# Kernel tuning notes

Measured on AMD Instinct MI355X. Metric: run time of the kernel, lower is better.

Reference implementation:

```python
import jax, jax.numpy as jnp
import numpy as np

NX, NU, ND = 512, 128, 64
BATCH, T = 256, 256


def setup_inputs() -> dict:
    key = jax.random.key(0)
    ks = jax.random.split(key, 7)
    return {
        "x": jax.random.normal(ks[0], (BATCH, NX), dtype=jnp.float32),
        "U": jax.random.normal(ks[1], (T, BATCH, NU), dtype=jnp.float32),
        "D": jax.random.normal(ks[2], (T, BATCH, ND), dtype=jnp.float32),
        "A_weight": jax.random.normal(ks[3], (NX, NX), dtype=jnp.float32),
        "A_scalar": jax.random.normal(ks[4], (NX, NX), dtype=jnp.float32),
        "B_weight": jax.random.normal(ks[5], (NX, NU), dtype=jnp.float32) * 0.05,
        "E_weight": jax.random.normal(ks[6], (NX, ND), dtype=jnp.float32) * 0.05,
    }


def _effective_W(weight, scalar):
    # (1 - 0.1*sigmoid(scalar)) * softmax(weight, axis=1), then transposed
    s_clamped = 1.0 - 0.1 * jax.nn.sigmoid(scalar)
    return (s_clamped * jax.nn.softmax(weight, axis=1)).T  # [nx, nx]


def reference(x, U, D, A_weight, A_scalar, B_weight, E_weight):
    W_eff = _effective_W(A_weight, A_scalar)            # hoisted: constant over time
    # Precompute input injections: [T, batch, nx]
    inj = jnp.einsum('tbu,xu->tbx', U, B_weight) + jnp.einsum('tbd,xd->tbx', D, E_weight)

    def step(x_prev, inj_t):
        x_new = x_prev @ W_eff + inj_t
        return x_new, x_new

    _, X = jax.lax.scan(step, x, inj)                   # X: [T, batch, nx]
    Y = X[:, :, -1]                                     # [T, batch]
    return X, Y
```

## Files before the change

kernel.cpp:

```cpp
#include <hip/hip_runtime.h>
#include <hip/hip_bf16.h>
#include <cstddef>

#define NXX 512
#define NUU 128
#define NDD 64
#define BB  256
#define TT  256
#define CL  8
#define NC  32
#define BS  (BB * NXX)
#define MS  (NXX * NXX)
#define LDK 32

typedef __attribute__((ext_vector_type(8))) short short8;
typedef __attribute__((ext_vector_type(8))) unsigned short ushort8;
typedef __attribute__((ext_vector_type(4))) unsigned short ushort4v;
typedef __attribute__((ext_vector_type(4))) float f32x4;

__device__ __forceinline__ unsigned short f2bf(float f) {
    union { float f; unsigned u; } v; v.f = f;
    unsigned r = v.u + 0x7FFFu + ((v.u >> 16) & 1u);
    return (unsigned short)(r >> 16);
}
__device__ __forceinline__ float bf2f(unsigned short h) {
    union { unsigned u; float f; } v; v.u = ((unsigned)h) << 16;
    return v.f;
}

enum StageKind { SK_BF16_NAT, SK_BF16_TRANS };

template<StageKind SK>
__device__ __forceinline__ void stage_tile(const void* src, int ld, int r0, int k0,
                                           unsigned short (*S)[LDK])
{
    const int tid = threadIdx.x;
    if constexpr (SK == SK_BF16_NAT) {
        const unsigned short* s = (const unsigned short*)src;
        const int wave = tid >> 6, lane = tid & 63;
#pragma unroll
        for (int i = 0; i < 2; ++i) {
            int rb = wave * 16 + i * 64;
            int r  = rb + (lane >> 2);
            int c  = (lane & 3) << 3;
            const unsigned short* g = s + (size_t)(r0 + r) * ld + k0 + c;
            __builtin_amdgcn_global_load_lds(
                (const __attribute__((address_space(1))) void*)g,
                (__attribute__((address_space(3))) void*)&S[rb][0],
                16, 0, 0);
        }
    } else {
        const unsigned short* s = (const unsigned short*)src;
#pragma unroll
        for (int i = 0; i < 2; ++i) {
            int idx = tid + i * 256;
            int m   = idx >> 4;
            int c   = (idx & 15) << 3;
            ushort8 v = *(const ushort8*)(s + (size_t)(k0 + m) * ld + r0 + c);
#pragma unroll
            for (int j = 0; j < 8; ++j) S[c + j][m] = v[j];
        }
    }
}

template<StageKind AK, StageKind BK>
__device__ __forceinline__ void gemm_mainloop(
    f32x4 (&acc)[4][4],
    const void* A, int lda, const void* B, int ldb,
    int K, int row0, int n0,
    unsigned short (*As)[LDK], unsigned short (*Bs)[LDK])
{
    const int tid  = threadIdx.x;
    const int lane = tid & 63;
    const int wave = tid >> 6;
    const int wm   = (wave >> 1) * 64;
    const int wn   = (wave & 1) * 64;
    const int l16  = lane & 15;
    const int quad = lane >> 4;

    for (int k0 = 0; k0 < K; k0 += 32) {
        __syncthreads();
        stage_tile<AK>(A, lda, row0, k0, As);
        stage_tile<BK>(B, ldb, n0,   k0, Bs);
        __syncthreads();
        short8 af[4], bfr[4];
#pragma unroll
        for (int f = 0; f < 4; ++f)
            af[f] = *(const short8*)&As[wm + f * 16 + l16][quad * 8];
#pragma unroll
        for (int f = 0; f < 4; ++f)
            bfr[f] = *(const short8*)&Bs[wn + f * 16 + l16][quad * 8];
#pragma unroll
        for (int fm = 0; fm < 4; ++fm)
#pragma unroll
            for (int fn = 0; fn < 4; ++fn)
                acc[fm][fn] = __builtin_amdgcn_mfma_f32_16x16x32_bf16(
                    af[fm], bfr[fn], acc[fm][fn], 0, 0, 0);
    }
}

__global__ __launch_bounds__(256) void k_weff(
    const float* __restrict__ Aw, const float* __restrict__ Asc,
    unsigned short* __restrict__ T1)
{
    const int n   = blockIdx.x;
    const int tid = threadIdx.x;
    const int lane = tid & 63, wave = tid >> 6;
    float v0 = Aw[(size_t)n * NXX + tid];
    float v1 = Aw[(size_t)n * NXX + 256 + tid];
    __shared__ float sred[4];
    float m = fmaxf(v0, v1);
#pragma unroll
    for (int off = 32; off; off >>= 1) m = fmaxf(m, __shfl_down(m, off));
    if (lane == 0) sred[wave] = m;
    __syncthreads();
    if (tid == 0) sred[0] = fmaxf(fmaxf(sred[0], sred[1]), fmaxf(sred[2], sred[3]));
    __syncthreads();
    const float mm = sred[0];
    __syncthreads();
    float e0 = expf(v0 - mm), e1 = expf(v1 - mm);
    float s = e0 + e1;
#pragma unroll
    for (int off = 32; off; off >>= 1) s += __shfl_down(s, off);
    if (lane == 0) sred[wave] = s;
    __syncthreads();
    if (tid == 0) sred[0] = sred[0] + sred[1] + sred[2] + sred[3];
    __syncthreads();
    const float inv = 1.0f / sred[0];
    float sc0 = 1.0f - 0.1f * (1.0f / (1.0f + expf(-Asc[(size_t)n * NXX + tid])));
    float sc1 = 1.0f - 0.1f * (1.0f / (1.0f + expf(-Asc[(size_t)n * NXX + 256 + tid])));
    unsigned short* out = T1 + (size_t)n * NXX;
    out[tid]       = f2bf(sc0 * e0 * inv);
    out[tid + 256] = f2bf(sc1 * e1 * inv);
}

__global__ __launch_bounds__(256) void k_prep(
    const float* __restrict__ Bw, const float* __restrict__ Ew,
    const float* __restrict__ x,
    unsigned short* __restrict__ Bwb, unsigned short* __restrict__ Ewb,
    unsigned short* __restrict__ G0)
{
    int i = (blockIdx.x * 256 + threadIdx.x) * 4;
    const float* src; unsigned short* dst; int k;
    if (i < 65536)       { src = Bw; dst = Bwb; k = i; }
    else if (i < 98304)  { src = Ew; dst = Ewb; k = i - 65536; }
    else                 { src = x;  dst = G0;  k = i - 98304; }
    float4 v = *(const float4*)(src + k);
    ushort4v h = { f2bf(v.x), f2bf(v.y), f2bf(v.z), f2bf(v.w) };
    *(ushort4v*)(dst + k) = h;
}

__global__ __launch_bounds__(256) void k_mulN(unsigned short* __restrict__ powb,
                                              int4 ns, int4 ts, int4 ds)
{
    const int z = blockIdx.z;
    const int an = (z == 0) ? ns.x : (z == 1) ? ns.y : (z == 2) ? ns.z : ns.w;
    const int at = (z == 0) ? ts.x : (z == 1) ? ts.y : (z == 2) ? ts.z : ts.w;
    const int ad = (z == 0) ? ds.x : (z == 1) ? ds.y : (z == 2) ? ds.z : ds.w;
    const unsigned short* A = powb + (size_t)an * MS;
    const unsigned short* B = powb + (size_t)at * MS;
    unsigned short*       D = powb + (size_t)ad * MS;
    __shared__ unsigned short As[128][LDK];
    __shared__ unsigned short Bs2[128][LDK];
    f32x4 acc[4][4] = {};
    const int row0 = blockIdx.y * 128, n0 = blockIdx.x * 128;
    gemm_mainloop<SK_BF16_NAT, SK_BF16_TRANS>(acc, A, NXX, B, NXX, NXX, row0, n0, As, Bs2);
    const int tid = threadIdx.x;
    const int lane = tid & 63, wave = tid >> 6;
    const int wm = (wave >> 1) * 64, wn = (wave & 1) * 64;
    const int l16 = lane & 15, quad = lane >> 4;
#pragma unroll
    for (int fm = 0; fm < 4; ++fm)
#pragma unroll
        for (int fn = 0; fn < 4; ++fn)
#pragma unroll
            for (int r = 0; r < 4; ++r) {
                int m = row0 + wm + fm * 16 + quad * 4 + r;
                int n = n0 + wn + fn * 16 + l16;
                D[(size_t)m * NXX + n] = f2bf(acc[fm][fn][r]);
            }
}

__global__ __launch_bounds__(256) void k_hs(
    const unsigned short* __restrict__ vsrc, unsigned short* __restrict__ vdst,
    const unsigned short* __restrict__ Am, int s)
{
    const int c = blockIdx.z;
    const int row0 = blockIdx.y * 128, n0 = blockIdx.x * 128;
    const int tid = threadIdx.x;
    if (c < s) {
        const unsigned short* sp = vsrc + (size_t)c * BS;
        unsigned short*       dp = vdst + (size_t)c * BS;
#pragma unroll
        for (int i = 0; i < 8; ++i) {
            int idx = tid + i * 256;
            int r = idx >> 4, cc = (idx & 15) << 3;
            *(ushort8*)(dp + (size_t)(row0 + r) * NXX + n0 + cc) =
                *(const ushort8*)(sp + (size_t)(row0 + r) * NXX + n0 + cc);
        }
        return;
    }
    __shared__ unsigned short As[128][LDK];
    __shared__ unsigned short Bs2[128][LDK];
    f32x4 acc[4][4] = {};
    gemm_mainloop<SK_BF16_NAT, SK_BF16_NAT>(acc, vsrc + (size_t)(c - s) * BS, NXX,
                                            Am, NXX, NXX, row0, n0, As, Bs2);
    const int lane = tid & 63, wave = tid >> 6;
    const int wm = (wave >> 1) * 64, wn = (wave & 1) * 64;
    const int l16 = lane & 15, quad = lane >> 4;
    const unsigned short* Cp = vsrc + (size_t)c * BS;
    unsigned short*       Dp = vdst + (size_t)c * BS;
#pragma unroll
    for (int fm = 0; fm < 4; ++fm)
#pragma unroll
        for (int fn = 0; fn < 4; ++fn)
#pragma unroll
            for (int r = 0; r < 4; ++r) {
                int m = row0 + wm + fm * 16 + quad * 4 + r;
                int n = n0 + wn + fn * 16 + l16;
                float v = acc[fm][fn][r] + bf2f(Cp[(size_t)m * NXX + n]);
                Dp[(size_t)m * NXX + n] = f2bf(v);
            }
}

__global__ __launch_bounds__(256) void k_xcorr(
    const unsigned short* __restrict__ vA, const unsigned short* __restrict__ powb,
    float* __restrict__ X, float* __restrict__ Y)
{
    const int t = blockIdx.z;
    const int c = t >> 3, j = t & 7;
    const int row0 = blockIdx.y * 128, n0 = blockIdx.x * 128;
    __shared__ unsigned short As[128][LDK];
    __shared__ unsigned short Bs2[128][LDK];
    f32x4 acc[4][4] = {};
    gemm_mainloop<SK_BF16_NAT, SK_BF16_NAT>(acc, vA + (size_t)c * BS, NXX,
                                            powb + (size_t)j * MS, NXX, NXX,
                                            row0, n0, As, Bs2);
    const int tid = threadIdx.x;
    const int lane = tid & 63, wave = tid >> 6;
    const int wm = (wave >> 1) * 64, wn = (wave & 1) * 64;
    const int l16 = lane & 15, quad = lane >> 4;
    float* Xt = X + (size_t)t * BB * NXX;
#pragma unroll
    for (int fm = 0; fm < 4; ++fm)
#pragma unroll
        for (int fn = 0; fn < 4; ++fn)
#pragma unroll
            for (int r = 0; r < 4; ++r) {
                int m = row0 + wm + fm * 16 + quad * 4 + r;
                int n = n0 + wn + fn * 16 + l16;
                float v = acc[fm][fn][r] + Xt[(size_t)m * NXX + n];
                Xt[(size_t)m * NXX + n] = v;
                if (n == NXX - 1) Y[(size_t)t * BB + m] = v;
            }
}

__global__ __launch_bounds__(1024, 4) void k_scanA(
    const float* __restrict__ U, const float* __restrict__ Dm,
    const unsigned short* __restrict__ Bwb, const unsigned short* __restrict__ Ewb,
    const unsigned short* __restrict__ Wt,
    unsigned short* __restrict__ Gout,
    float* __restrict__ X)
{
    const int c   = blockIdx.x;
    const int r0  = blockIdx.y * 32;
    const int tid = threadIdx.x;
    const int lane = tid & 63, wave = tid >> 6;
    const int l16 = lane & 15, quad = lane >> 4;

    __shared__ unsigned short Sb[32][520];
    __shared__ unsigned short Ub[32][136];
    __shared__ unsigned short Db[32][72];

    int woff[2], bwoff[2], ewoff[2];
#pragma unroll
    for (int g = 0; g < 2; ++g) {
        int n = wave * 32 + g * 16 + l16;
        woff[g]  = n * NXX + quad * 8;
        bwoff[g] = n * NUU + quad * 8;
        ewoff[g] = n * NDD + quad * 8;
    }

    f32x4 acc[2][2];

    for (int j = 0; j < CL; ++j) {
        const int t = c * CL + j;
        {
            int row = tid >> 5;
            int uc  = (tid & 31) * 4;
            const float* up = U + ((size_t)t * BB + r0 + row) * NUU + uc;
            float4 a0 = *(const float4*)(up);
            ushort4v h0 = { f2bf(a0.x), f2bf(a0.y), f2bf(a0.z), f2bf(a0.w) };
            *(ushort4v*)&Ub[row][uc] = h0;
            int dc = (tid & 31) * 2;
            const float* dp = Dm + ((size_t)t * BB + r0 + row) * NDD + dc;
            float2 b0 = *(const float2*)(dp);
            unsigned pk = (unsigned)f2bf(b0.x) | ((unsigned)f2bf(b0.y) << 16);
            *(unsigned*)&Db[row][dc] = pk;
        }
        __syncthreads();

#pragma unroll
        for (int f = 0; f < 2; ++f)
#pragma unroll
            for (int g = 0; g < 2; ++g) acc[f][g] = (f32x4){0.f, 0.f, 0.f, 0.f};

#pragma unroll
        for (int kk = 0; kk < 4; ++kk) {
            short8 a0 = *(const short8*)&Ub[l16][kk * 32 + quad * 8];
            short8 a1 = *(const short8*)&Ub[16 + l16][kk * 32 + quad * 8];
#pragma unroll
            for (int g = 0; g < 2; ++g) {
                short8 b = *(const short8*)(Bwb + bwoff[g] + kk * 32);
                acc[0][g] = __builtin_amdgcn_mfma_f32_16x16x32_bf16(a0, b, acc[0][g], 0, 0, 0);
                acc[1][g] = __builtin_amdgcn_mfma_f32_16x16x32_bf16(a1, b, acc[1][g], 0, 0, 0);
            }
        }
#pragma unroll
        for (int kk = 0; kk < 2; ++kk) {
            short8 a0 = *(const short8*)&Db[l16][kk * 32 + quad * 8];
            short8 a1 = *(const short8*)&Db[16 + l16][kk * 32 + quad * 8];
#pragma unroll
            for (int g = 0; g < 2; ++g) {
                short8 b = *(const short8*)(Ewb + ewoff[g] + kk * 32);
                acc[0][g] = __builtin_amdgcn_mfma_f32_16x16x32_bf16(a0, b, acc[0][g], 0, 0, 0);
                acc[1][g] = __builtin_amdgcn_mfma_f32_16x16x32_bf16(a1, b, acc[1][g], 0, 0, 0);
            }
        }
        if (j > 0) {
#pragma unroll
            for (int kk = 0; kk < 16; ++kk) {
                short8 a0 = *(const short8*)&Sb[l16][kk * 32 + quad * 8];
                short8 a1 = *(const short8*)&Sb[16 + l16][kk * 32 + quad * 8];
#pragma unroll
                for (int g = 0; g < 2; ++g) {
                    short8 b = *(const short8*)(Wt + woff[g] + kk * 32);
                    acc[0][g] = __builtin_amdgcn_mfma_f32_16x16x32_bf16(a0, b, acc[0][g], 0, 0, 0);
                    acc[1][g] = __builtin_amdgcn_mfma_f32_16x16x32_bf16(a1, b, acc[1][g], 0, 0, 0);
                }
            }
        }
        __syncthreads();

#pragma unroll
        for (int f = 0; f < 2; ++f)
#pragma unroll
            for (int g = 0; g < 2; ++g) {
                int n = wave * 32 + g * 16 + l16;
#pragma unroll
                for (int rr = 0; rr < 4; ++rr) {
                    int mr = f * 16 + quad * 4 + rr;
                    float v = acc[f][g][rr];
                    unsigned short hb = f2bf(v);
                    Sb[mr][n] = hb;
                    X[((size_t)t * BB + r0 + mr) * NXX + n] = v;
                    if (j == CL - 1)
                        Gout[((size_t)(c + 1) * BB + r0 + mr) * NXX + n] = hb;
                }
            }
    }
}

extern "C" void kernel_launch(void* const* d_in, const int* in_sizes, int n_in,
                              void* d_out, int out_size, void* d_ws, size_t ws_size,
                              hipStream_t stream)
{
    const float* x   = (const float*)d_in[0];
    const float* U   = (const float*)d_in[1];
    const float* Dm  = (const float*)d_in[2];
    const float* Aw  = (const float*)d_in[3];
    const float* Asc = (const float*)d_in[4];
    const float* Bw  = (const float*)d_in[5];
    const float* Ew  = (const float*)d_in[6];

    float* Xout = (float*)d_out;
    float* Yout = Xout + (size_t)TT * BB * NXX;

    unsigned short* powb = (unsigned short*)d_ws;
    unsigned short* Bwb  = powb + (size_t)12 * MS;
    unsigned short* Ewb  = Bwb + (size_t)NXX * NUU;
    unsigned short* Gbuf = Ewb + (size_t)NXX * NDD;
    unsigned short* vA   = Gbuf + (size_t)(NC + 1) * BS;
    unsigned short* vB   = vA + (size_t)NC * BS;

    dim3 blk(256);
    dim3 blkScan(1024);

    k_weff<<<dim3(512), blk, 0, stream>>>(Aw, Asc, powb);
    k_prep<<<dim3(224), blk, 0, stream>>>(Bw, Ew, x, Bwb, Ewb, Gbuf);

    k_mulN<<<dim3(4, 4, 1), blk, 0, stream>>>(powb,
        make_int4(0, 0, 0, 0), make_int4(0, 0, 0, 0), make_int4(1, 0, 0, 0));
    k_mulN<<<dim3(4, 4, 2), blk, 0, stream>>>(powb,
        make_int4(1, 1, 0, 0), make_int4(0, 1, 0, 0), make_int4(2, 3, 0, 0));
    k_mulN<<<dim3(4, 4, 4), blk, 0, stream>>>(powb,
        make_int4(3, 3, 3, 3), make_int4(0, 1, 2, 3), make_int4(4, 5, 6, 7));
    k_mulN<<<dim3(4, 4, 1), blk, 0, stream>>>(powb,
        make_int4(7, 0, 0, 0), make_int4(7, 0, 0, 0), make_int4(8, 0, 0, 0));
    k_mulN<<<dim3(4, 4, 1), blk, 0, stream>>>(powb,
        make_int4(8, 0, 0, 0), make_int4(8, 0, 0, 0), make_int4(9, 0, 0, 0));
    k_mulN<<<dim3(4, 4, 1), blk, 0, stream>>>(powb,
        make_int4(9, 0, 0, 0), make_int4(9, 0, 0, 0), make_int4(10, 0, 0, 0));
    k_mulN<<<dim3(4, 4, 1), blk, 0, stream>>>(powb,
        make_int4(10, 0, 0, 0), make_int4(10, 0, 0, 0), make_int4(11, 0, 0, 0));

    k_scanA<<<dim3(NC, 8), blkScan, 0, stream>>>(
        U, Dm, Bwb, Ewb, powb, Gbuf, Xout);

    k_hs<<<dim3(4, 2, NC), blk, 0, stream>>>(Gbuf, vA, powb + (size_t)7 * MS, 1);
    k_hs<<<dim3(4, 2, NC), blk, 0, stream>>>(vA, vB, powb + (size_t)8 * MS, 2);
    k_hs<<<dim3(4, 2, NC), blk, 0, stream>>>(vB, vA, powb + (size_t)9 * MS, 4);
    k_hs<<<dim3(4, 2, NC), blk, 0, stream>>>(vA, vB, powb + (size_t)10 * MS, 8);
    k_hs<<<dim3(4, 2, NC), blk, 0, stream>>>(vB, vA, powb + (size_t)11 * MS, 16);

    k_xcorr<<<dim3(4, 2, TT), blk, 0, stream>>>(vA, powb, Xout, Yout);
}
```

Baseline: 663.6 us.

## Double-buffer GEMM and scan LDS tiles, fuse matrix squarings into scan passes

The GEMM mainloop now double-buffers its LDS tiles and prefetches the next K-slice while MFMAs run on the current one, which halves the barriers per iteration. The scan kernel double-buffers its state and U/D tiles and prefetches the next timestep's inputs. The serial chain of W^8..W^128 squaring launches is folded into the Hillis-Steele passes as extra blocks. Each squaring runs one pass before the power it produces is consumed, so the small dependent launches overlap with useful work. The cost is twice the LDS per block, which may lower occupancy.

```diff
diff --git a/kernel.cpp b/kernel.cpp
--- a/kernel.cpp
+++ b/kernel.cpp
@@ -30,45 +30,46 @@
 
 enum StageKind { SK_BF16_NAT, SK_BF16_TRANS };
 
-template<StageKind SK>
-__device__ __forceinline__ void stage_tile(const void* src, int ld, int r0, int k0,
-                                           unsigned short (*S)[LDK])
-{
-    const int tid = threadIdx.x;
-    if constexpr (SK == SK_BF16_NAT) {
-        const unsigned short* s = (const unsigned short*)src;
-        const int wave = tid >> 6, lane = tid & 63;
-#pragma unroll
-        for (int i = 0; i < 2; ++i) {
-            int rb = wave * 16 + i * 64;
-            int r  = rb + (lane >> 2);
-            int c  = (lane & 3) << 3;
-            const unsigned short* g = s + (size_t)(r0 + r) * ld + k0 + c;
-            __builtin_amdgcn_global_load_lds(
-                (const __attribute__((address_space(1))) void*)g,
-                (__attribute__((address_space(3))) void*)&S[rb][0],
-                16, 0, 0);
-        }
-    } else {
-        const unsigned short* s = (const unsigned short*)src;
-#pragma unroll
-        for (int i = 0; i < 2; ++i) {
-            int idx = tid + i * 256;
-            int m   = idx >> 4;
-            int c   = (idx & 15) << 3;
-            ushort8 v = *(const ushort8*)(s + (size_t)(k0 + m) * ld + r0 + c);
-#pragma unroll
-            for (int j = 0; j < 8; ++j) S[c + j][m] = v[j];
-        }
-    }
+__device__ __forceinline__ void stage_nat(const unsigned short* s, int ld, int r0,
+                                          int k0, unsigned short (*S)[LDK])
+{
+    const int tid = threadIdx.x;
+    const int wave = tid >> 6, lane = tid & 63;
+#pragma unroll
+    for (int i = 0; i < 2; ++i) {
+        int rb = wave * 16 + i * 64;
+        int r  = rb + (lane >> 2);
+        int c  = (lane & 3) << 3;
+        const unsigned short* g = s + (size_t)(r0 + r) * ld + k0 + c;
+        __builtin_amdgcn_global_load_lds(
+            (const __attribute__((address_space(1))) void*)g,
+            (__attribute__((address_space(3))) void*)&S[rb][0],
+            16, 0, 0);
+    }
+}
+__device__ __forceinline__ ushort8 ldT(const unsigned short* s, int ld, int r0,
+                                       int k0, int i)
+{
+    int idx = threadIdx.x + i * 256;
+    int m   = idx >> 4;
+    int c   = (idx & 15) << 3;
+    return *(const ushort8*)(s + (size_t)(k0 + m) * ld + r0 + c);
+}
+__device__ __forceinline__ void wrT(ushort8 v, int i, unsigned short (*S)[LDK])
+{
+    int idx = threadIdx.x + i * 256;
+    int m   = idx >> 4;
+    int c   = (idx & 15) << 3;
+#pragma unroll
+    for (int j = 0; j < 8; ++j) S[c + j][m] = v[j];
 }
 
 template<StageKind AK, StageKind BK>
-__device__ __forceinline__ void gemm_mainloop(
+__device__ __forceinline__ void gemm2_mainloop(
     f32x4 (&acc)[4][4],
     const void* A, int lda, const void* B, int ldb,
     int K, int row0, int n0,
-    unsigned short (*As)[LDK], unsigned short (*Bs)[LDK])
+    unsigned short (*As)[128][LDK], unsigned short (*Bs)[128][LDK])
 {
     const int tid  = threadIdx.x;
     const int lane = tid & 63;
@@ -77,25 +78,44 @@
     const int wn   = (wave & 1) * 64;
     const int l16  = lane & 15;
     const int quad = lane >> 4;
-
-    for (int k0 = 0; k0 < K; k0 += 32) {
-        __syncthreads();
-        stage_tile<AK>(A, lda, row0, k0, As);
-        stage_tile<BK>(B, ldb, n0,   k0, Bs);
-        __syncthreads();
+    const unsigned short* Ap = (const unsigned short*)A;
+    const unsigned short* Bp = (const unsigned short*)B;
+    const int NT = K >> 5;
+
+    if constexpr (AK == SK_BF16_NAT) stage_nat(Ap, lda, row0, 0, As[0]);
+    else { wrT(ldT(Ap, lda, row0, 0, 0), 0, As[0]); wrT(ldT(Ap, lda, row0, 0, 1), 1, As[0]); }
+    if constexpr (BK == SK_BF16_NAT) stage_nat(Bp, ldb, n0, 0, Bs[0]);
+    else { wrT(ldT(Bp, ldb, n0, 0, 0), 0, Bs[0]); wrT(ldT(Bp, ldb, n0, 0, 1), 1, Bs[0]); }
+    __syncthreads();
+
+    for (int t = 0; t < NT; ++t) {
+        const int cur = t & 1, nxt = cur ^ 1;
+        const int k1  = (t + 1) << 5;
+        ushort8 ta0, ta1, tb0, tb1;
+        if (t + 1 < NT) {
+            if constexpr (AK == SK_BF16_NAT) stage_nat(Ap, lda, row0, k1, As[nxt]);
+            else { ta0 = ldT(Ap, lda, row0, k1, 0); ta1 = ldT(Ap, lda, row0, k1, 1); }
+            if constexpr (BK == SK_BF16_NAT) stage_nat(Bp, ldb, n0, k1, Bs[nxt]);
+            else { tb0 = ldT(Bp, ldb, n0, k1, 0); tb1 = ldT(Bp, ldb, n0, k1, 1); }
+        }
         short8 af[4], bfr[4];
 #pragma unroll
         for (int f = 0; f < 4; ++f)
-            af[f] = *(const short8*)&As[wm + f * 16 + l16][quad * 8];
+            af[f] = *(const short8*)&As[cur][wm + f * 16 + l16][quad * 8];
 #pragma unroll
         for (int f = 0; f < 4; ++f)
-            bfr[f] = *(const short8*)&Bs[wn + f * 16 + l16][quad * 8];
+            bfr[f] = *(const short8*)&Bs[cur][wn + f * 16 + l16][quad * 8];
 #pragma unroll
         for (int fm = 0; fm < 4; ++fm)
 #pragma unroll
             for (int fn = 0; fn < 4; ++fn)
                 acc[fm][fn] = __builtin_amdgcn_mfma_f32_16x16x32_bf16(
                     af[fm], bfr[fn], acc[fm][fn], 0, 0, 0);
+        if (t + 1 < NT) {
+            if constexpr (AK == SK_BF16_TRANS) { wrT(ta0, 0, As[nxt]); wrT(ta1, 1, As[nxt]); }
+            if constexpr (BK == SK_BF16_TRANS) { wrT(tb0, 0, Bs[nxt]); wrT(tb1, 1, Bs[nxt]); }
+        }
+        __syncthreads();
     }
 }
 
@@ -160,11 +180,11 @@
     const unsigned short* A = powb + (size_t)an * MS;
     const unsigned short* B = powb + (size_t)at * MS;
     unsigned short*       D = powb + (size_t)ad * MS;
-    __shared__ unsigned short As[128][LDK];
-    __shared__ unsigned short Bs2[128][LDK];
+    __shared__ unsigned short As[2][128][LDK];
+    __shared__ unsigned short Bs2[2][128][LDK];
     f32x4 acc[4][4] = {};
     const int row0 = blockIdx.y * 128, n0 = blockIdx.x * 128;
-    gemm_mainloop<SK_BF16_NAT, SK_BF16_TRANS>(acc, A, NXX, B, NXX, NXX, row0, n0, As, Bs2);
+    gemm2_mainloop<SK_BF16_NAT, SK_BF16_TRANS>(acc, A, NXX, B, NXX, NXX, row0, n0, As, Bs2);
     const int tid = threadIdx.x;
     const int lane = tid & 63, wave = tid >> 6;
     const int wm = (wave >> 1) * 64, wn = (wave & 1) * 64;
@@ -181,13 +201,41 @@
             }
 }
 
-__global__ __launch_bounds__(256) void k_hs(
+__global__ __launch_bounds__(256) void k_hs_sq(
     const unsigned short* __restrict__ vsrc, unsigned short* __restrict__ vdst,
-    const unsigned short* __restrict__ Am, int s)
-{
-    const int c = blockIdx.z;
+    const unsigned short* __restrict__ Am, int s,
+    unsigned short* __restrict__ powb, int sqa, int sqd)
+{
+    const int z = blockIdx.z;
+    const int tid = threadIdx.x;
+    __shared__ unsigned short As[2][128][LDK];
+    __shared__ unsigned short Bs2[2][128][LDK];
+    const int lane = tid & 63, wave = tid >> 6;
+    const int wm = (wave >> 1) * 64, wn = (wave & 1) * 64;
+    const int l16 = lane & 15, quad = lane >> 4;
+
+    if (z >= NC) {
+        const unsigned short* Aq = powb + (size_t)sqa * MS;
+        unsigned short*       Dq = powb + (size_t)sqd * MS;
+        const int row0 = (blockIdx.y + 2 * (z - NC)) * 128;
+        const int n0   = blockIdx.x * 128;
+        f32x4 acc[4][4] = {};
+        gemm2_mainloop<SK_BF16_NAT, SK_BF16_TRANS>(acc, Aq, NXX, Aq, NXX, NXX, row0, n0, As, Bs2);
+#pragma unroll
+        for (int fm = 0; fm < 4; ++fm)
+#pragma unroll
+            for (int fn = 0; fn < 4; ++fn)
+#pragma unroll
+                for (int r = 0; r < 4; ++r) {
+                    int m = row0 + wm + fm * 16 + quad * 4 + r;
+                    int n = n0 + wn + fn * 16 + l16;
+                    Dq[(size_t)m * NXX + n] = f2bf(acc[fm][fn][r]);
+                }
+        return;
+    }
+
+    const int c = z;
     const int row0 = blockIdx.y * 128, n0 = blockIdx.x * 128;
-    const int tid = threadIdx.x;
     if (c < s) {
         const unsigned short* sp = vsrc + (size_t)c * BS;
         unsigned short*       dp = vdst + (size_t)c * BS;
@@ -200,14 +248,9 @@
         }
         return;
     }
-    __shared__ unsigned short As[128][LDK];
-    __shared__ unsigned short Bs2[128][LDK];
     f32x4 acc[4][4] = {};
-    gemm_mainloop<SK_BF16_NAT, SK_BF16_NAT>(acc, vsrc + (size_t)(c - s) * BS, NXX,
-                                            Am, NXX, NXX, row0, n0, As, Bs2);
-    const int lane = tid & 63, wave = tid >> 6;
-    const int wm = (wave >> 1) * 64, wn = (wave & 1) * 64;
-    const int l16 = lane & 15, quad = lane >> 4;
+    gemm2_mainloop<SK_BF16_NAT, SK_BF16_NAT>(acc, vsrc + (size_t)(c - s) * BS, NXX,
+                                             Am, NXX, NXX, row0, n0, As, Bs2);
     const unsigned short* Cp = vsrc + (size_t)c * BS;
     unsigned short*       Dp = vdst + (size_t)c * BS;
 #pragma unroll
@@ -230,12 +273,12 @@
     const int t = blockIdx.z;
     const int c = t >> 3, j = t & 7;
     const int row0 = blockIdx.y * 128, n0 = blockIdx.x * 128;
-    __shared__ unsigned short As[128][LDK];
-    __shared__ unsigned short Bs2[128][LDK];
+    __shared__ unsigned short As[2][128][LDK];
+    __shared__ unsigned short Bs2[2][128][LDK];
     f32x4 acc[4][4] = {};
-    gemm_mainloop<SK_BF16_NAT, SK_BF16_NAT>(acc, vA + (size_t)c * BS, NXX,
-                                            powb + (size_t)j * MS, NXX, NXX,
-                                            row0, n0, As, Bs2);
+    gemm2_mainloop<SK_BF16_NAT, SK_BF16_NAT>(acc, vA + (size_t)c * BS, NXX,
+                                             powb + (size_t)j * MS, NXX, NXX,
+                                             row0, n0, As, Bs2);
     const int tid = threadIdx.x;
     const int lane = tid & 63, wave = tid >> 6;
     const int wm = (wave >> 1) * 64, wn = (wave & 1) * 64;
@@ -268,9 +311,24 @@
     const int lane = tid & 63, wave = tid >> 6;
     const int l16 = lane & 15, quad = lane >> 4;
 
-    __shared__ unsigned short Sb[32][520];
-    __shared__ unsigned short Ub[32][136];
-    __shared__ unsigned short Db[32][72];
+    __shared__ unsigned short Sb[2][32][520];
+    __shared__ unsigned short Ub[2][32][136];
+    __shared__ unsigned short Db[2][32][72];
+
+    const int srow = tid >> 5;
+    const int su   = (tid & 31) * 4;
+    const int sd   = (tid & 31) * 2;
+
+    {
+        const float* up = U + ((size_t)(c * CL) * BB + r0 + srow) * NUU + su;
+        float4 a0 = *(const float4*)up;
+        ushort4v h0 = { f2bf(a0.x), f2bf(a0.y), f2bf(a0.z), f2bf(a0.w) };
+        *(ushort4v*)&Ub[0][srow][su] = h0;
+        const float* dp = Dm + ((size_t)(c * CL) * BB + r0 + srow) * NDD + sd;
+        float2 b0 = *(const float2*)dp;
+        unsigned pk = (unsigned)f2bf(b0.x) | ((unsigned)f2bf(b0.y) << 16);
+        *(unsigned*)&Db[0][srow][sd] = pk;
+    }
 
     int woff[2], bwoff[2], ewoff[2];
 #pragma unroll
@@ -284,22 +342,17 @@
     f32x4 acc[2][2];
 
     for (int j = 0; j < CL; ++j) {
-        const int t = c * CL + j;
-        {
-            int row = tid >> 5;
-            int uc  = (tid & 31) * 4;
-            const float* up = U + ((size_t)t * BB + r0 + row) * NUU + uc;
-            float4 a0 = *(const float4*)(up);
-            ushort4v h0 = { f2bf(a0.x), f2bf(a0.y), f2bf(a0.z), f2bf(a0.w) };
-            *(ushort4v*)&Ub[row][uc] = h0;
-            int dc = (tid & 31) * 2;
-            const float* dp = Dm + ((size_t)t * BB + r0 + row) * NDD + dc;
-            float2 b0 = *(const float2*)(dp);
-            unsigned pk = (unsigned)f2bf(b0.x) | ((unsigned)f2bf(b0.y) << 16);
-            *(unsigned*)&Db[row][dc] = pk;
-        }
+        const int t   = c * CL + j;
+        const int cur = j & 1, nxt = cur ^ 1;
+
         __syncthreads();
 
+        float4 pu; float2 pd;
+        if (j + 1 < CL) {
+            pu = *(const float4*)(U + ((size_t)(t + 1) * BB + r0 + srow) * NUU + su);
+            pd = *(const float2*)(Dm + ((size_t)(t + 1) * BB + r0 + srow) * NDD + sd);
+        }
+
 #pragma unroll
         for (int f = 0; f < 2; ++f)
 #pragma unroll
@@ -307,8 +360,8 @@
 
 #pragma unroll
         for (int kk = 0; kk < 4; ++kk) {
-            short8 a0 = *(const short8*)&Ub[l16][kk * 32 + quad * 8];
-            short8 a1 = *(const short8*)&Ub[16 + l16][kk * 32 + quad * 8];
+            short8 a0 = *(const short8*)&Ub[cur][l16][kk * 32 + quad * 8];
+            short8 a1 = *(const short8*)&Ub[cur][16 + l16][kk * 32 + quad * 8];
 #pragma unroll
             for (int g = 0; g < 2; ++g) {
                 short8 b = *(const short8*)(Bwb + bwoff[g] + kk * 32);
@@ -318,8 +371,8 @@
         }
 #pragma unroll
         for (int kk = 0; kk < 2; ++kk) {
-            short8 a0 = *(const short8*)&Db[l16][kk * 32 + quad * 8];
-            short8 a1 = *(const short8*)&Db[16 + l16][kk * 32 + quad * 8];
+            short8 a0 = *(const short8*)&Db[cur][l16][kk * 32 + quad * 8];
+            short8 a1 = *(const short8*)&Db[cur][16 + l16][kk * 32 + quad * 8];
 #pragma unroll
             for (int g = 0; g < 2; ++g) {
                 short8 b = *(const short8*)(Ewb + ewoff[g] + kk * 32);
@@ -330,8 +383,8 @@
         if (j > 0) {
 #pragma unroll
             for (int kk = 0; kk < 16; ++kk) {
-                short8 a0 = *(const short8*)&Sb[l16][kk * 32 + quad * 8];
-                short8 a1 = *(const short8*)&Sb[16 + l16][kk * 32 + quad * 8];
+                short8 a0 = *(const short8*)&Sb[cur][l16][kk * 32 + quad * 8];
+                short8 a1 = *(const short8*)&Sb[cur][16 + l16][kk * 32 + quad * 8];
 #pragma unroll
                 for (int g = 0; g < 2; ++g) {
                     short8 b = *(const short8*)(Wt + woff[g] + kk * 32);
@@ -340,7 +393,6 @@
                 }
             }
         }
-        __syncthreads();
 
 #pragma unroll
         for (int f = 0; f < 2; ++f)
@@ -352,12 +404,19 @@
                     int mr = f * 16 + quad * 4 + rr;
                     float v = acc[f][g][rr];
                     unsigned short hb = f2bf(v);
-                    Sb[mr][n] = hb;
+                    Sb[nxt][mr][n] = hb;
                     X[((size_t)t * BB + r0 + mr) * NXX + n] = v;
                     if (j == CL - 1)
                         Gout[((size_t)(c + 1) * BB + r0 + mr) * NXX + n] = hb;
                 }
             }
+
+        if (j + 1 < CL) {
+            ushort4v h0 = { f2bf(pu.x), f2bf(pu.y), f2bf(pu.z), f2bf(pu.w) };
+            *(ushort4v*)&Ub[nxt][srow][su] = h0;
+            unsigned pk = (unsigned)f2bf(pd.x) | ((unsigned)f2bf(pd.y) << 16);
+            *(unsigned*)&Db[nxt][srow][sd] = pk;
+        }
     }
 }
 
@@ -395,23 +454,20 @@
         make_int4(1, 1, 0, 0), make_int4(0, 1, 0, 0), make_int4(2, 3, 0, 0));
     k_mulN<<<dim3(4, 4, 4), blk, 0, stream>>>(powb,
         make_int4(3, 3, 3, 3), make_int4(0, 1, 2, 3), make_int4(4, 5, 6, 7));
-    k_mulN<<<dim3(4, 4, 1), blk, 0, stream>>>(powb,
-        make_int4(7, 0, 0, 0), make_int4(7, 0, 0, 0), make_int4(8, 0, 0, 0));
-    k_mulN<<<dim3(4, 4, 1), blk, 0, stream>>>(powb,
-        make_int4(8, 0, 0, 0), make_int4(8, 0, 0, 0), make_int4(9, 0, 0, 0));
-    k_mulN<<<dim3(4, 4, 1), blk, 0, stream>>>(powb,
-        make_int4(9, 0, 0, 0), make_int4(9, 0, 0, 0), make_int4(10, 0, 0, 0));
-    k_mulN<<<dim3(4, 4, 1), blk, 0, stream>>>(powb,
-        make_int4(10, 0, 0, 0), make_int4(10, 0, 0, 0), make_int4(11, 0, 0, 0));
 
     k_scanA<<<dim3(NC, 8), blkScan, 0, stream>>>(
         U, Dm, Bwb, Ewb, powb, Gbuf, Xout);
 
-    k_hs<<<dim3(4, 2, NC), blk, 0, stream>>>(Gbuf, vA, powb + (size_t)7 * MS, 1);
-    k_hs<<<dim3(4, 2, NC), blk, 0, stream>>>(vA, vB, powb + (size_t)8 * MS, 2);
-    k_hs<<<dim3(4, 2, NC), blk, 0, stream>>>(vB, vA, powb + (size_t)9 * MS, 4);
-    k_hs<<<dim3(4, 2, NC), blk, 0, stream>>>(vA, vB, powb + (size_t)10 * MS, 8);
-    k_hs<<<dim3(4, 2, NC), blk, 0, stream>>>(vB, vA, powb + (size_t)11 * MS, 16);
+    k_hs_sq<<<dim3(4, 2, NC + 2), blk, 0, stream>>>(Gbuf, vA, powb + (size_t)7 * MS, 1,
+                                                    powb, 7, 8);
+    k_hs_sq<<<dim3(4, 2, NC + 2), blk, 0, stream>>>(vA, vB, powb + (size_t)8 * MS, 2,
+                                                    powb, 8, 9);
+    k_hs_sq<<<dim3(4, 2, NC + 2), blk, 0, stream>>>(vB, vA, powb + (size_t)9 * MS, 4,
+                                                    powb, 9, 10);
+    k_hs_sq<<<dim3(4, 2, NC + 2), blk, 0, stream>>>(vA, vB, powb + (size_t)10 * MS, 8,
+                                                    powb, 10, 11);
+    k_hs_sq<<<dim3(4, 2, NC), blk, 0, stream>>>(vB, vA, powb + (size_t)11 * MS, 16,
+                                                powb, 0, 0);
 
     k_xcorr<<<dim3(4, 2, TT), blk, 0, stream>>>(vA, powb, Xout, Yout);
 }
```

Result: faster. 611.4 us (-7.9%).
